# Optimization experiments

Hardware: AMD Instinct MI355X
Metric: run time of the kernel (lower is better)

The kernel has to match this reference:

```python
import jax, jax.numpy as jnp
import numpy as np

V, E, H, T, B, D, L = 32000, 512, 512, 128, 4, 4, 2
C0, C1 = 2000, 10000          # adaptive softmax cutoffs
NT = T - D + 1


def setup_inputs() -> dict:
    key = jax.random.key(0)
    ks = jax.random.split(key, 18)
    s = 0.02
    x = jax.random.randint(ks[0], (B, T), 1, V)
    lengths = jnp.sort(jax.random.randint(ks[1], (B,), D, T + 1))[::-1]
    lengths = lengths.at[0].set(T)
    # graph predictor output: per-layer attention matrices [B, L, T, T]
    G = jax.nn.softmax(jax.random.normal(ks[2], (B, L, T, T)), axis=-1)
    emb = (jax.random.normal(ks[3], (V, E)) * s).at[0].set(0.0)  # padding_idx=0
    enc_w_ih = jax.random.normal(ks[4], (L, 3 * H, H)) * s
    enc_w_hh = jax.random.normal(ks[5], (L, 3 * H, H)) * s
    enc_b_ih = jnp.zeros((L, 3 * H))
    enc_b_hh = jnp.zeros((L, 3 * H))
    dec_w_ih = jax.random.normal(ks[6], (3 * H, E)) * s
    dec_w_hh = jax.random.normal(ks[7], (3 * H, H)) * s
    dec_b_ih = jnp.zeros((3 * H,))
    dec_b_hh = jnp.zeros((3 * H,))
    head_w = jax.random.normal(ks[8], (C0 + 2, H)) * s
    t0_proj = jax.random.normal(ks[9], (H // 4, H)) * s
    t0_out = jax.random.normal(ks[10], (C1 - C0, H // 4)) * s
    t1_proj = jax.random.normal(ks[11], (H // 16, H)) * s
    t1_out = jax.random.normal(ks[12], (V - C1, H // 16)) * s
    return dict(x=x, lengths=lengths, G=G, emb=emb,
                enc_w_ih=enc_w_ih, enc_w_hh=enc_w_hh, enc_b_ih=enc_b_ih, enc_b_hh=enc_b_hh,
                dec_w_ih=dec_w_ih, dec_w_hh=dec_w_hh, dec_b_ih=dec_b_ih, dec_b_hh=dec_b_hh,
                head_w=head_w, t0_proj=t0_proj, t0_out=t0_out, t1_proj=t1_proj, t1_out=t1_out)


def gru_step(xt, h, w_ih, w_hh, b_ih, b_hh):
    """torch nn.GRU/GRUCell math; works on arbitrary leading dims."""
    gi = xt @ w_ih.T + b_ih
    gh = h @ w_hh.T + b_hh
    i_r, i_z, i_n = jnp.split(gi, 3, axis=-1)
    h_r, h_z, h_n = jnp.split(gh, 3, axis=-1)
    r = jax.nn.sigmoid(i_r + h_r)
    z = jax.nn.sigmoid(i_z + h_z)
    n = jnp.tanh(i_n + r * h_n)
    return (1.0 - z) * n + z * h


def adaptive_log_prob(h, head_w, t0_proj, t0_out, t1_proj, t1_out):
    """torch AdaptiveLogSoftmaxWithLoss.log_prob: h [N,H] -> [N,V]."""
    head_lp = jax.nn.log_softmax(h @ head_w.T, axis=-1)                      # [N, C0+2]
    lp0 = head_lp[:, C0:C0 + 1] + jax.nn.log_softmax((h @ t0_proj.T) @ t0_out.T, axis=-1)
    lp1 = head_lp[:, C0 + 1:C0 + 2] + jax.nn.log_softmax((h @ t1_proj.T) @ t1_out.T, axis=-1)
    return jnp.concatenate([head_lp[:, :C0], lp0, lp1], axis=-1)


def reference(x, lengths, G, emb, enc_w_ih, enc_w_hh, enc_b_ih, enc_b_hh,
              dec_w_ih, dec_w_hh, dec_b_ih, dec_b_hh,
              head_w, t0_proj, t0_out, t1_proj, t1_out):
    b = x.shape[0]
    input_f = emb[x]                      # [B,T,E] (dropout p=0)
    embedded = input_f
    # ---- encoder: graph-weighted aggregation + GRUCell per layer ----
    for l in range(enc_w_ih.shape[0]):
        wgt = jnp.einsum('bji,bjd->bid', G[:, l], input_f)   # G_l^T @ input_f
        input_f = gru_step(wgt, input_f, enc_w_ih[l], enc_w_hh[l], enc_b_ih[l], enc_b_hh[l])
    # ---- decoder: length-D GRU window per start position t ----
    t_idx = jnp.arange(NT)
    d_idx = jnp.arange(D)
    tok_idx = jnp.broadcast_to(t_idx[None, :, None] + d_idx[None, None, :] - 1, (b, NT, D))
    tok_idx = tok_idx.at[:, 0, 0].set(lengths - 1)           # t=0,d=0 uses embedded[lengths-1]
    wins = jnp.take_along_axis(embedded, tok_idx.reshape(b, -1)[:, :, None], axis=1)
    wins = wins.reshape(b, NT, D, E)
    h0 = input_f[:, :NT, :]                                  # [B,NT,H]
    def step(h, xd):
        hn = gru_step(xd, h, dec_w_ih, dec_w_hh, dec_b_ih, dec_b_hh)
        return hn, hn
    _, hs = jax.lax.scan(step, h0, jnp.moveaxis(wins, 2, 0))  # [D,B,NT,H]
    hs = jnp.moveaxis(hs, 0, 2)                               # [B,NT,D,H]
    # pad_packed_sequence zeros hidden beyond per-row lens = min(lengths - t, D)
    valid = (t_idx[None, :, None] + d_idx[None, None, :]) < lengths[:, None, None]
    hs = jnp.where(valid[..., None], hs, 0.0)
    lp = adaptive_log_prob(hs.reshape(-1, H), head_w, t0_proj, t0_out, t1_proj, t1_out)
    lp = lp.reshape(b, NT, D, V)
    # batch rows with lengths <= t were excluded and F.pad'ed with zeros
    row_valid = t_idx[None, :] < lengths[:, None]
    lp = jnp.where(row_valid[:, :, None, None], lp, 0.0)
    return lp.reshape(b, NT * D, V)
```

## Files before the change

kernel.cpp:

```cpp
#include <hip/hip_runtime.h>
#include <hip/hip_bf16.h>

typedef __hip_bfloat16 bf16;
typedef __attribute__((ext_vector_type(8))) short short8v;
typedef __attribute__((ext_vector_type(4))) float float4v;

#define V_    32000
#define E_    512
#define H_    512
#define T_    128
#define B_    4
#define D_    4
#define L_    2
#define C0_   2000
#define C1_   10000
#define NT_   125
#define NROW_ 2000
#define NH_   2002
#define NTOTC 2162
#define NSLOT 252

__device__ __forceinline__ float bf2f(bf16 v) { return __bfloat162float(v); }
__device__ __forceinline__ unsigned short f2bfu(float f) {
    bf16 h = __float2bfloat16(f);
    union { bf16 h; unsigned short u; } cv; cv.h = h; return cv.u;
}
__device__ __forceinline__ float ubf2f(unsigned short u) {
    return __uint_as_float(((unsigned)u) << 16);
}
__device__ __forceinline__ float ld1(const void* p, size_t i, int bf) {
    return bf ? bf2f(((const bf16*)p)[i]) : ((const float*)p)[i];
}
__device__ __forceinline__ void st1(void* p, size_t i, int bf, float v) {
    if (bf) ((unsigned short*)p)[i] = f2bfu(v);
    else    ((float*)p)[i] = v;
}

__device__ __forceinline__ void lse_push(float z, float& m, float& s) {
    if (z <= m) { s += __expf(z - m); }
    else        { s = s * __expf(m - z) + 1.0f; m = z; }
}
__device__ __forceinline__ void lse_merge(float m2, float s2, float& m, float& s) {
    float mm = fmaxf(m, m2);
    s = s * __expf(m - mm) + s2 * __expf(m2 - mm);
    m = mm;
}

__global__ void k_detect(const void* __restrict__ G, int* __restrict__ flag) {
    int t = threadIdx.x;
    float s32 = 0.0f;
    for (int k = t; k < 128; k += 64) s32 += ((const float*)G)[k];
    for (int off = 32; off; off >>= 1) s32 += __shfl_down(s32, off);
    if (t == 0) {
        float e32 = fabsf(s32 - 1.0f);
        *flag = (e32 < 0.05f) ? 0 : 1;
    }
}

struct ConvArgs {
    const void* src[9];
    unsigned int off[10];
};
__global__ void k_wconv(ConvArgs a, unsigned short* __restrict__ wb,
                        const int* __restrict__ flagp) {
    const int bf = *flagp;
    unsigned int total = a.off[9];
    for (unsigned int i = blockIdx.x * 256 + threadIdx.x; i < total;
         i += gridDim.x * 256) {
        int seg = 0;
        while (i >= a.off[seg + 1]) seg++;
        wb[i] = f2bfu(ld1(a.src[seg], i - a.off[seg], bf));
    }
}

__global__ void k_embed(const int* __restrict__ x, const void* __restrict__ emb,
                        float* __restrict__ embedded, float* __restrict__ f0,
                        unsigned short* __restrict__ f0b,
                        const int* __restrict__ flagp) {
    const int bf = *flagp;
    int i = blockIdx.x * 256 + threadIdx.x;
    int bt = i >> 9, e = i & 511;
    int tok = x[bt];
    float v = ld1(emb, (size_t)tok * E_ + e, bf);
    embedded[i] = v; f0[i] = v; f0b[i] = f2bfu(v);
}

__global__ void k_wgt(const void* __restrict__ G, const float* __restrict__ f,
                      unsigned short* __restrict__ wgtb, int l,
                      const int* __restrict__ flagp) {
    const int bf = *flagp;
    int i = blockIdx.x * 256 + threadIdx.x;
    int e = i & 511;
    int bi = i >> 9;
    int b = bi >> 7, ip = bi & 127;
    size_t gbase = ((size_t)(b * L_ + l) * T_ * T_) + ip;
    const float* fb = f + (size_t)b * T_ * E_ + e;
    float acc = 0.0f;
    #pragma unroll 4
    for (int j = 0; j < T_; ++j)
        acc = fmaf(ld1(G, gbase + (size_t)j * T_, bf), fb[(size_t)j * E_], acc);
    wgtb[i] = f2bfu(acc);
}

template<int MODE>
__global__ void k_gemm(const unsigned short* __restrict__ A,
                       const unsigned short* __restrict__ Bw,
                       int M, int N, int K, int Nlse,
                       float* __restrict__ Zg, int zcolOff,
                       const void* __restrict__ bias, int biasOff,
                       void* __restrict__ out, int outColOff,
                       float* __restrict__ stats,
                       unsigned short* __restrict__ p0b,
                       unsigned short* __restrict__ p1b,
                       float* __restrict__ lsep, int slotBase,
                       const int* __restrict__ flagp) {
    const int bf = *flagp;
    const int bx = blockIdx.x, by = blockIdx.y;
    const int m0 = by * 128, n0 = bx * 128;
    const int t = threadIdx.x;
    const int wave = t >> 6, lane = t & 63;
    const int wm = wave >> 1, wn = wave & 1;
    const int quad = lane >> 4, l16 = lane & 15;

    __shared__ __align__(16) unsigned short As[128 * 40];
    __shared__ __align__(16) unsigned short Bs[128 * 40];
    __shared__ float pm[128][2], ps[128][2];

    float4v acc[4][4];
    #pragma unroll
    for (int mi = 0; mi < 4; ++mi)
        #pragma unroll
        for (int ni = 0; ni < 4; ++ni)
            acc[mi][ni] = (float4v){0.f, 0.f, 0.f, 0.f};

    for (int k0 = 0; k0 < K; k0 += 32) {
        if (k0) __syncthreads();
        #pragma unroll
        for (int i = 0; i < 2; ++i) {
            int idx = t + i * 256;
            int row = idx >> 2, seg = idx & 3;
            uint4 av = {0u, 0u, 0u, 0u};
            int gm = m0 + row;
            if (gm < M) av = *(const uint4*)(A + (size_t)gm * K + k0 + seg * 8);
            *(uint4*)(&As[row * 40 + seg * 8]) = av;
            uint4 bv = {0u, 0u, 0u, 0u};
            int gn = n0 + row;
            if (gn < N) bv = *(const uint4*)(Bw + (size_t)gn * K + k0 + seg * 8);
            *(uint4*)(&Bs[row * 40 + seg * 8]) = bv;
        }
        __syncthreads();
        short8v af[4], bfv[4];
        #pragma unroll
        for (int mi = 0; mi < 4; ++mi)
            af[mi] = *(const short8v*)(As + (wm * 64 + mi * 16 + l16) * 40 + quad * 8);
        #pragma unroll
        for (int ni = 0; ni < 4; ++ni)
            bfv[ni] = *(const short8v*)(Bs + (wn * 64 + ni * 16 + l16) * 40 + quad * 8);
        #pragma unroll
        for (int mi = 0; mi < 4; ++mi)
            #pragma unroll
            for (int ni = 0; ni < 4; ++ni)
                acc[mi][ni] = __builtin_amdgcn_mfma_f32_16x16x32_bf16(
                    af[mi], bfv[ni], acc[mi][ni], 0, 0, 0);
    }

    #pragma unroll
    for (int mi = 0; mi < 4; ++mi) {
        #pragma unroll
        for (int r = 0; r < 4; ++r) {
            int grow = m0 + wm * 64 + mi * 16 + quad * 4 + r;
            if (grow >= M) continue;
            #pragma unroll
            for (int ni = 0; ni < 4; ++ni) {
                int gcol = n0 + wn * 64 + ni * 16 + l16;
                float v = acc[mi][ni][r];
                if (MODE == 0) {
                    if (gcol < N)
                        Zg[(size_t)grow * 3072 + zcolOff + gcol] =
                            v + ld1(bias, biasOff + gcol, bf);
                } else if (MODE == 1) {
                    if (gcol < C0_)        st1(out, (size_t)grow * V_ + gcol, bf, v);
                    else if (gcol < NH_)   stats[grow * 8 + 2 + (gcol - C0_)] = v;
                    else if (gcol < 2130)  p0b[grow * 128 + (gcol - NH_)] = f2bfu(v);
                    else if (gcol < NTOTC) p1b[grow * 32 + (gcol - 2130)] = f2bfu(v);
                } else {
                    if (gcol < N)
                        st1(out, (size_t)grow * V_ + outColOff + gcol, bf, v);
                }
            }
        }
    }

    if (MODE != 0) {
        #pragma unroll
        for (int mi = 0; mi < 4; ++mi) {
            #pragma unroll
            for (int r = 0; r < 4; ++r) {
                float m = -1e30f, s = 0.0f;
                #pragma unroll
                for (int ni = 0; ni < 4; ++ni) {
                    int gcol = n0 + wn * 64 + ni * 16 + l16;
                    if (gcol < Nlse) lse_push(acc[mi][ni][r], m, s);
                }
                #pragma unroll
                for (int off = 1; off < 16; off <<= 1) {
                    float m2 = __shfl_xor(m, off), s2 = __shfl_xor(s, off);
                    lse_merge(m2, s2, m, s);
                }
                if (l16 == 0) {
                    int rl = wm * 64 + mi * 16 + quad * 4 + r;
                    pm[rl][wn] = m; ps[rl][wn] = s;
                }
            }
        }
        __syncthreads();
        if (t < 128) {
            int grow = m0 + t;
            if (grow < M) {
                float m = pm[t][0], s = ps[t][0];
                lse_merge(pm[t][1], ps[t][1], m, s);
                float* dst = lsep + ((size_t)grow * NSLOT + slotBase + bx) * 2;
                dst[0] = m; dst[1] = s;
            }
        }
    }
}

__device__ __forceinline__ float gru_out(const float* grow, int k, float h) {
    float i_r = grow[k], i_z = grow[512 + k], i_n = grow[1024 + k];
    float h_r = grow[1536 + k], h_z = grow[2048 + k], h_n = grow[2560 + k];
    float r = 1.0f / (1.0f + __expf(-(i_r + h_r)));
    float z = 1.0f / (1.0f + __expf(-(i_z + h_z)));
    float n = tanhf(i_n + r * h_n);
    return (1.0f - z) * n + z * h;
}

__global__ void k_apply_enc(const float* __restrict__ gates,
                            const float* __restrict__ hprev,
                            float* __restrict__ hnext,
                            unsigned short* __restrict__ hnextb) {
    int i = blockIdx.x * 256 + threadIdx.x;
    int row = i >> 9, k = i & 511;
    float v = gru_out(gates + (size_t)row * 3072, k, hprev[i]);
    hnext[i] = v; hnextb[i] = f2bfu(v);
}

__global__ void k_h0(const float* __restrict__ ffin, float* __restrict__ hdec,
                     unsigned short* __restrict__ hdecb) {
    int i = blockIdx.x * 256 + threadIdx.x;
    int row = i >> 9, e = i & 511;
    int b = row / NT_, t = row - b * NT_;
    float v = ffin[((size_t)(b * T_ + t) << 9) + e];
    hdec[i] = v; hdecb[i] = f2bfu(v);
}

__global__ void k_win(const float* __restrict__ embedded,
                      const int* __restrict__ lengths,
                      unsigned short* __restrict__ winb, int d) {
    int i = blockIdx.x * 256 + threadIdx.x;
    int row = i >> 9, e = i & 511;
    int b = row / NT_, t = row - b * NT_;
    int tok = (d == 0 && t == 0) ? (lengths[b] - 1) : (t + d - 1);
    winb[i] = f2bfu(embedded[((size_t)(b * T_ + tok) << 9) + e]);
}

__global__ void k_apply_dec(const float* __restrict__ gates,
                            float* __restrict__ hdec,
                            unsigned short* __restrict__ hdecb,
                            unsigned short* __restrict__ hsb,
                            const int* __restrict__ lengths, int d) {
    int i = blockIdx.x * 256 + threadIdx.x;
    int row = i >> 9, k = i & 511;
    int b = row / NT_, t = row - b * NT_;
    float hn = gru_out(gates + (size_t)row * 3072, k, hdec[i]);
    hdec[i] = hn; hdecb[i] = f2bfu(hn);
    bool valid = (t + d) < lengths[b];
    hsb[(((size_t)row * D_ + d) << 9) + k] = valid ? f2bfu(hn) : (unsigned short)0;
}

__global__ void k_corr2(const float* __restrict__ lsep, const float* __restrict__ stats,
                        float* __restrict__ corr) {
    int r = blockIdx.x * 256 + threadIdx.x;
    if (r >= NROW_) return;
    const float* P = lsep + (size_t)r * NSLOT * 2;
    float m = -1e30f, s = 0.0f;
    for (int i = 0; i < 17; ++i)  lse_merge(P[2 * i], P[2 * i + 1], m, s);
    float ch = m + logf(s);
    float lp0 = stats[r * 8 + 2] - ch;
    float lp1 = stats[r * 8 + 3] - ch;
    m = -1e30f; s = 0.0f;
    for (int i = 17; i < 80; ++i) lse_merge(P[2 * i], P[2 * i + 1], m, s);
    float ct0 = m + logf(s);
    m = -1e30f; s = 0.0f;
    for (int i = 80; i < 252; ++i) lse_merge(P[2 * i], P[2 * i + 1], m, s);
    float ct1 = m + logf(s);
    corr[r * 4 + 0] = ch;
    corr[r * 4 + 1] = ct0 - lp0;
    corr[r * 4 + 2] = ct1 - lp1;
}

__global__ void k_final(void* __restrict__ out, const float* __restrict__ corr,
                        const int* __restrict__ lengths, const int* __restrict__ flagp) {
    const int bf = *flagp;
    size_t vec = (size_t)blockIdx.x * 256 + threadIdx.x;
    size_t base = vec << 3;
    int r = (int)(base / V_);
    int c = (int)(base - (size_t)r * V_);
    int b = r / 500;
    int t = (r - b * 500) >> 2;
    if (t >= lengths[b]) {
        if (bf) { uint4 z = {0u,0u,0u,0u}; *(uint4*)((unsigned short*)out + base) = z; }
        else { float4 z = {0.f,0.f,0.f,0.f};
               float4* p = (float4*)((float*)out + base); p[0] = z; p[1] = z; }
        return;
    }
    float cr = (c < C0_) ? corr[r * 4 + 0] : ((c < C1_) ? corr[r * 4 + 1] : corr[r * 4 + 2]);
    if (bf) {
        uint4 u = *(const uint4*)((const unsigned short*)out + base);
        unsigned us[8] = {u.x & 0xffffu, u.x >> 16, u.y & 0xffffu, u.y >> 16,
                          u.z & 0xffffu, u.z >> 16, u.w & 0xffffu, u.w >> 16};
        unsigned short o[8];
        #pragma unroll
        for (int q = 0; q < 8; ++q)
            o[q] = f2bfu(ubf2f((unsigned short)us[q]) - cr);
        uint4 w;
        w.x = (unsigned)o[0] | ((unsigned)o[1] << 16);
        w.y = (unsigned)o[2] | ((unsigned)o[3] << 16);
        w.z = (unsigned)o[4] | ((unsigned)o[5] << 16);
        w.w = (unsigned)o[6] | ((unsigned)o[7] << 16);
        *(uint4*)((unsigned short*)out + base) = w;
    } else {
        float4* p = (float4*)((float*)out + base);
        float4 a0 = p[0], a1 = p[1];
        a0.x -= cr; a0.y -= cr; a0.z -= cr; a0.w -= cr;
        a1.x -= cr; a1.y -= cr; a1.z -= cr; a1.w -= cr;
        p[0] = a0; p[1] = a1;
    }
}

#define OFF_EMB    0u
#define OFF_FA     262144u
#define OFF_FB     524288u
#define OFF_FAB    786432u
#define OFF_FBB    917504u
#define OFF_WGTB   1048576u
#define OFF_GATES  1179648u
#define OFF_HDEC   2752512u
#define OFF_HDECB  3008512u
#define OFF_WINB   3136512u
#define OFF_HSB    3264512u
#define OFF_P0B    3776512u
#define OFF_P1B    3904512u
#define OFF_STATS  3936512u
#define OFF_CORR   3952512u
#define OFF_LSEP   3960512u
#define OFF_WB     4968512u
#define OFF_FLAG   8745264u

#define WO_ENCIH   0u
#define WO_ENCHH   1572864u
#define WO_DECIH   3145728u
#define WO_DECHH   3932160u
#define WO_W1      4718592u
#define WO_T0O     5825536u
#define WO_T1O     6849536u
#define WO_END     7553504u

extern "C" void kernel_launch(void* const* d_in, const int* in_sizes, int n_in,
                              void* d_out, int out_size, void* d_ws, size_t ws_size,
                              hipStream_t stream) {
    (void)in_sizes; (void)n_in; (void)out_size; (void)ws_size;
    const int*  x        = (const int*)d_in[0];
    const int*  lengths  = (const int*)d_in[1];
    const void* G        = d_in[2];
    const void* emb      = d_in[3];
    const void* enc_w_ih = d_in[4];
    const void* enc_w_hh = d_in[5];
    const void* enc_b_ih = d_in[6];
    const void* enc_b_hh = d_in[7];
    const void* dec_w_ih = d_in[8];
    const void* dec_w_hh = d_in[9];
    const void* dec_b_ih = d_in[10];
    const void* dec_b_hh = d_in[11];
    const void* head_w   = d_in[12];
    const void* t0_proj  = d_in[13];
    const void* t0_out   = d_in[14];
    const void* t1_proj  = d_in[15];
    const void* t1_out   = d_in[16];

    float* ws = (float*)d_ws;
    float* embedded = ws + OFF_EMB;
    float* fA    = ws + OFF_FA;
    float* fB    = ws + OFF_FB;
    unsigned short* fAb  = (unsigned short*)(ws + OFF_FAB);
    unsigned short* fBb  = (unsigned short*)(ws + OFF_FBB);
    unsigned short* wgtb = (unsigned short*)(ws + OFF_WGTB);
    float* gates = ws + OFF_GATES;
    float* hdec  = ws + OFF_HDEC;
    unsigned short* hdecb = (unsigned short*)(ws + OFF_HDECB);
    unsigned short* winb  = (unsigned short*)(ws + OFF_WINB);
    unsigned short* hsb   = (unsigned short*)(ws + OFF_HSB);
    unsigned short* p0b   = (unsigned short*)(ws + OFF_P0B);
    unsigned short* p1b   = (unsigned short*)(ws + OFF_P1B);
    float* stats = ws + OFF_STATS;
    float* corr  = ws + OFF_CORR;
    float* lsep  = ws + OFF_LSEP;
    unsigned short* WB = (unsigned short*)(ws + OFF_WB);
    int* flagp = (int*)(ws + OFF_FLAG);
    void* out = d_out;

    k_detect<<<1, 64, 0, stream>>>(G, flagp);

    ConvArgs ca;
    ca.src[0] = enc_w_ih; ca.src[1] = enc_w_hh; ca.src[2] = dec_w_ih;
    ca.src[3] = dec_w_hh; ca.src[4] = head_w;   ca.src[5] = t0_proj;
    ca.src[6] = t1_proj;  ca.src[7] = t0_out;   ca.src[8] = t1_out;
    ca.off[0] = WO_ENCIH; ca.off[1] = WO_ENCHH; ca.off[2] = WO_DECIH;
    ca.off[3] = WO_DECHH; ca.off[4] = WO_W1;
    ca.off[5] = WO_W1 + 2002u * 512u;
    ca.off[6] = WO_W1 + 2130u * 512u;
    ca.off[7] = WO_T0O;   ca.off[8] = WO_T1O;   ca.off[9] = WO_END;
    k_wconv<<<4096, 256, 0, stream>>>(ca, WB, flagp);

    k_embed<<<1024, 256, 0, stream>>>(x, emb, embedded, fA, fAb, flagp);

    k_wgt<<<1024, 256, 0, stream>>>(G, fA, wgtb, 0, flagp);
    k_gemm<0><<<dim3(12, 4), 256, 0, stream>>>(wgtb, WB + WO_ENCIH, 512, 1536, 512, 0,
        gates, 0, enc_b_ih, 0, nullptr, 0, nullptr, nullptr, nullptr, nullptr, 0, flagp);
    k_gemm<0><<<dim3(12, 4), 256, 0, stream>>>(fAb, WB + WO_ENCHH, 512, 1536, 512, 0,
        gates, 1536, enc_b_hh, 0, nullptr, 0, nullptr, nullptr, nullptr, nullptr, 0, flagp);
    k_apply_enc<<<1024, 256, 0, stream>>>(gates, fA, fB, fBb);

    k_wgt<<<1024, 256, 0, stream>>>(G, fB, wgtb, 1, flagp);
    k_gemm<0><<<dim3(12, 4), 256, 0, stream>>>(wgtb, WB + WO_ENCIH + 786432u, 512, 1536, 512, 0,
        gates, 0, enc_b_ih, 1536, nullptr, 0, nullptr, nullptr, nullptr, nullptr, 0, flagp);
    k_gemm<0><<<dim3(12, 4), 256, 0, stream>>>(fBb, WB + WO_ENCHH + 786432u, 512, 1536, 512, 0,
        gates, 1536, enc_b_hh, 1536, nullptr, 0, nullptr, nullptr, nullptr, nullptr, 0, flagp);
    k_apply_enc<<<1024, 256, 0, stream>>>(gates, fB, fA, fAb);

    k_h0<<<1000, 256, 0, stream>>>(fA, hdec, hdecb);
    for (int d = 0; d < D_; ++d) {
        k_win<<<1000, 256, 0, stream>>>(embedded, lengths, winb, d);
        k_gemm<0><<<dim3(12, 4), 256, 0, stream>>>(winb, WB + WO_DECIH, 500, 1536, 512, 0,
            gates, 0, dec_b_ih, 0, nullptr, 0, nullptr, nullptr, nullptr, nullptr, 0, flagp);
        k_gemm<0><<<dim3(12, 4), 256, 0, stream>>>(hdecb, WB + WO_DECHH, 500, 1536, 512, 0,
            gates, 1536, dec_b_hh, 0, nullptr, 0, nullptr, nullptr, nullptr, nullptr, 0, flagp);
        k_apply_dec<<<1000, 256, 0, stream>>>(gates, hdec, hdecb, hsb, lengths, d);
    }

    k_gemm<1><<<dim3(17, 16), 256, 0, stream>>>(hsb, WB + WO_W1, NROW_, NTOTC, 512, NH_,
        nullptr, 0, nullptr, 0, out, 0, stats, p0b, p1b, lsep, 0, flagp);
    k_gemm<2><<<dim3(63, 16), 256, 0, stream>>>(p0b, WB + WO_T0O, NROW_, 8000, 128, 8000,
        nullptr, 0, nullptr, 0, out, C0_, stats, nullptr, nullptr, lsep, 17, flagp);
    k_gemm<3><<<dim3(172, 16), 256, 0, stream>>>(p1b, WB + WO_T1O, NROW_, 22000, 32, 22000,
        nullptr, 0, nullptr, 0, out, C1_, stats, nullptr, nullptr, lsep, 80, flagp);

    k_corr2<<<8, 256, 0, stream>>>(lsep, stats, corr);
    k_final<<<31250, 256, 0, stream>>>(out, corr, lengths, flagp);
}
```

Before: 925.4 us.

## Recompute logit GEMMs after LSE instead of read-modify-write output pass

```diff
diff --git a/kernel.cpp b/kernel.cpp
--- a/kernel.cpp
+++ b/kernel.cpp
@@ -24,9 +24,6 @@
 __device__ __forceinline__ unsigned short f2bfu(float f) {
     bf16 h = __float2bfloat16(f);
     union { bf16 h; unsigned short u; } cv; cv.h = h; return cv.u;
-}
-__device__ __forceinline__ float ubf2f(unsigned short u) {
-    return __uint_as_float(((unsigned)u) << 16);
 }
 __device__ __forceinline__ float ld1(const void* p, size_t i, int bf) {
     return bf ? bf2f(((const bf16*)p)[i]) : ((const float*)p)[i];
@@ -102,19 +99,31 @@
     wgtb[i] = f2bfu(acc);
 }
 
+struct GemmP {
+    const unsigned short* A0;
+    const unsigned short* A1;
+    const unsigned short* W;
+    unsigned long long w1off;
+    int M, N, K, Nlse;
+    float* Zg; int ldz; int zcol1;
+    const void* bias0; const void* bias1; int boff;
+    void* out; int outColOff;
+    float* stats;
+    unsigned short* p0b;
+    unsigned short* p1b;
+    float* lsep; int slotBase;
+    const float* corr;
+    const int* lengths;
+    const int* flagp;
+};
+
 template<int MODE>
-__global__ void k_gemm(const unsigned short* __restrict__ A,
-                       const unsigned short* __restrict__ Bw,
-                       int M, int N, int K, int Nlse,
-                       float* __restrict__ Zg, int zcolOff,
-                       const void* __restrict__ bias, int biasOff,
-                       void* __restrict__ out, int outColOff,
-                       float* __restrict__ stats,
-                       unsigned short* __restrict__ p0b,
-                       unsigned short* __restrict__ p1b,
-                       float* __restrict__ lsep, int slotBase,
-                       const int* __restrict__ flagp) {
-    const int bf = *flagp;
+__global__ void k_gemm(GemmP p) {
+    const int bf = *p.flagp;
+    const int zsel = blockIdx.z;
+    const unsigned short* A  = zsel ? p.A1 : p.A0;
+    const unsigned short* Bw = p.W + (zsel ? p.w1off : 0ull);
+    const int M = p.M, N = p.N, K = p.K;
     const int bx = blockIdx.x, by = blockIdx.y;
     const int m0 = by * 128, n0 = bx * 128;
     const int t = threadIdx.x;
@@ -164,34 +173,64 @@
                     af[mi], bfv[ni], acc[mi][ni], 0, 0, 0);
     }
 
-    #pragma unroll
-    for (int mi = 0; mi < 4; ++mi) {
-        #pragma unroll
-        for (int r = 0; r < 4; ++r) {
-            int grow = m0 + wm * 64 + mi * 16 + quad * 4 + r;
-            if (grow >= M) continue;
+    if (MODE == 0) {
+        const void* bias = zsel ? p.bias1 : p.bias0;
+        const int zcol = zsel ? p.zcol1 : 0;
+        #pragma unroll
+        for (int mi = 0; mi < 4; ++mi)
             #pragma unroll
-            for (int ni = 0; ni < 4; ++ni) {
-                int gcol = n0 + wn * 64 + ni * 16 + l16;
-                float v = acc[mi][ni][r];
-                if (MODE == 0) {
+            for (int r = 0; r < 4; ++r) {
+                int grow = m0 + wm * 64 + mi * 16 + quad * 4 + r;
+                if (grow >= M) continue;
+                #pragma unroll
+                for (int ni = 0; ni < 4; ++ni) {
+                    int gcol = n0 + wn * 64 + ni * 16 + l16;
                     if (gcol < N)
-                        Zg[(size_t)grow * 3072 + zcolOff + gcol] =
-                            v + ld1(bias, biasOff + gcol, bf);
-                } else if (MODE == 1) {
-                    if (gcol < C0_)        st1(out, (size_t)grow * V_ + gcol, bf, v);
-                    else if (gcol < NH_)   stats[grow * 8 + 2 + (gcol - C0_)] = v;
-                    else if (gcol < 2130)  p0b[grow * 128 + (gcol - NH_)] = f2bfu(v);
-                    else if (gcol < NTOTC) p1b[grow * 32 + (gcol - 2130)] = f2bfu(v);
-                } else {
-                    if (gcol < N)
-                        st1(out, (size_t)grow * V_ + outColOff + gcol, bf, v);
+                        p.Zg[(size_t)grow * p.ldz + zcol + gcol] =
+                            acc[mi][ni][r] + ld1(bias, p.boff + gcol, bf);
                 }
             }
-        }
+    } else if (MODE == 1) {
+        #pragma unroll
+        for (int mi = 0; mi < 4; ++mi)
+            #pragma unroll
+            for (int r = 0; r < 4; ++r) {
+                int grow = m0 + wm * 64 + mi * 16 + quad * 4 + r;
+                if (grow >= M) continue;
+                #pragma unroll
+                for (int ni = 0; ni < 4; ++ni) {
+                    int gcol = n0 + wn * 64 + ni * 16 + l16;
+                    float v = acc[mi][ni][r];
+                    if (gcol >= C0_ && gcol < NH_) p.stats[grow * 8 + 2 + (gcol - C0_)] = v;
+                    else if (gcol >= NH_ && gcol < 2130) p.p0b[grow * 128 + (gcol - NH_)] = f2bfu(v);
+                    else if (gcol >= 2130 && gcol < NTOTC) p.p1b[grow * 32 + (gcol - 2130)] = f2bfu(v);
+                }
+            }
+    } else if (MODE >= 3) {
+        const int crIdx = MODE - 3;
+        #pragma unroll
+        for (int mi = 0; mi < 4; ++mi)
+            #pragma unroll
+            for (int r = 0; r < 4; ++r) {
+                int grow = m0 + wm * 64 + mi * 16 + quad * 4 + r;
+                if (grow >= M) continue;
+                int b = grow / 500;
+                int tt = (grow - b * 500) >> 2;
+                bool valid = tt < p.lengths[b];
+                float cr = p.corr[grow * 4 + crIdx];
+                #pragma unroll
+                for (int ni = 0; ni < 4; ++ni) {
+                    int gcol = n0 + wn * 64 + ni * 16 + l16;
+                    if (gcol < N) {
+                        float v = valid ? (acc[mi][ni][r] - cr) : 0.0f;
+                        st1(p.out, (size_t)grow * V_ + p.outColOff + gcol, bf, v);
+                    }
+                }
+            }
     }
 
-    if (MODE != 0) {
+    if (MODE == 1 || MODE == 2) {
+        const int Nlse = p.Nlse;
         #pragma unroll
         for (int mi = 0; mi < 4; ++mi) {
             #pragma unroll
@@ -219,16 +258,15 @@
             if (grow < M) {
                 float m = pm[t][0], s = ps[t][0];
                 lse_merge(pm[t][1], ps[t][1], m, s);
-                float* dst = lsep + ((size_t)grow * NSLOT + slotBase + bx) * 2;
+                float* dst = p.lsep + ((size_t)grow * NSLOT + p.slotBase + bx) * 2;
                 dst[0] = m; dst[1] = s;
             }
         }
     }
 }
 
-__device__ __forceinline__ float gru_out(const float* grow, int k, float h) {
-    float i_r = grow[k], i_z = grow[512 + k], i_n = grow[1024 + k];
-    float h_r = grow[1536 + k], h_z = grow[2048 + k], h_n = grow[2560 + k];
+__device__ __forceinline__ float gru2(float i_r, float i_z, float i_n,
+                                      float h_r, float h_z, float h_n, float h) {
     float r = 1.0f / (1.0f + __expf(-(i_r + h_r)));
     float z = 1.0f / (1.0f + __expf(-(i_z + h_z)));
     float n = tanhf(i_n + r * h_n);
@@ -241,7 +279,9 @@
                             unsigned short* __restrict__ hnextb) {
     int i = blockIdx.x * 256 + threadIdx.x;
     int row = i >> 9, k = i & 511;
-    float v = gru_out(gates + (size_t)row * 3072, k, hprev[i]);
+    const float* g = gates + (size_t)row * 3072;
+    float v = gru2(g[k], g[512 + k], g[1024 + k],
+                   g[1536 + k], g[2048 + k], g[2560 + k], hprev[i]);
     hnext[i] = v; hnextb[i] = f2bfu(v);
 }
 
@@ -254,17 +294,20 @@
     hdec[i] = v; hdecb[i] = f2bfu(v);
 }
 
-__global__ void k_win(const float* __restrict__ embedded,
-                      const int* __restrict__ lengths,
-                      unsigned short* __restrict__ winb, int d) {
+__global__ void k_winall(const float* __restrict__ embedded,
+                         const int* __restrict__ lengths,
+                         unsigned short* __restrict__ winb) {
     int i = blockIdx.x * 256 + threadIdx.x;
-    int row = i >> 9, e = i & 511;
+    int e = i & 511;
+    int wr = i >> 9;
+    int d = wr / 500, row = wr - d * 500;
     int b = row / NT_, t = row - b * NT_;
     int tok = (d == 0 && t == 0) ? (lengths[b] - 1) : (t + d - 1);
     winb[i] = f2bfu(embedded[((size_t)(b * T_ + tok) << 9) + e]);
 }
 
-__global__ void k_apply_dec(const float* __restrict__ gates,
+__global__ void k_apply_dec(const float* __restrict__ gih,
+                            const float* __restrict__ ghh,
                             float* __restrict__ hdec,
                             unsigned short* __restrict__ hdecb,
                             unsigned short* __restrict__ hsb,
@@ -272,7 +315,10 @@
     int i = blockIdx.x * 256 + threadIdx.x;
     int row = i >> 9, k = i & 511;
     int b = row / NT_, t = row - b * NT_;
-    float hn = gru_out(gates + (size_t)row * 3072, k, hdec[i]);
+    const float* gi = gih + (size_t)(d * 500 + row) * 1536;
+    const float* gh = ghh + (size_t)row * 1536;
+    float hn = gru2(gi[k], gi[512 + k], gi[1024 + k],
+                    gh[k], gh[512 + k], gh[1024 + k], hdec[i]);
     hdec[i] = hn; hdecb[i] = f2bfu(hn);
     bool valid = (t + d) < lengths[b];
     hsb[(((size_t)row * D_ + d) << 9) + k] = valid ? f2bfu(hn) : (unsigned short)0;
@@ -299,45 +345,6 @@
     corr[r * 4 + 2] = ct1 - lp1;
 }
 
-__global__ void k_final(void* __restrict__ out, const float* __restrict__ corr,
-                        const int* __restrict__ lengths, const int* __restrict__ flagp) {
-    const int bf = *flagp;
-    size_t vec = (size_t)blockIdx.x * 256 + threadIdx.x;
-    size_t base = vec << 3;
-    int r = (int)(base / V_);
-    int c = (int)(base - (size_t)r * V_);
-    int b = r / 500;
-    int t = (r - b * 500) >> 2;
-    if (t >= lengths[b]) {
-        if (bf) { uint4 z = {0u,0u,0u,0u}; *(uint4*)((unsigned short*)out + base) = z; }
-        else { float4 z = {0.f,0.f,0.f,0.f};
-               float4* p = (float4*)((float*)out + base); p[0] = z; p[1] = z; }
-        return;
-    }
-    float cr = (c < C0_) ? corr[r * 4 + 0] : ((c < C1_) ? corr[r * 4 + 1] : corr[r * 4 + 2]);
-    if (bf) {
-        uint4 u = *(const uint4*)((const unsigned short*)out + base);
-        unsigned us[8] = {u.x & 0xffffu, u.x >> 16, u.y & 0xffffu, u.y >> 16,
-                          u.z & 0xffffu, u.z >> 16, u.w & 0xffffu, u.w >> 16};
-        unsigned short o[8];
-        #pragma unroll
-        for (int q = 0; q < 8; ++q)
-            o[q] = f2bfu(ubf2f((unsigned short)us[q]) - cr);
-        uint4 w;
-        w.x = (unsigned)o[0] | ((unsigned)o[1] << 16);
-        w.y = (unsigned)o[2] | ((unsigned)o[3] << 16);
-        w.z = (unsigned)o[4] | ((unsigned)o[5] << 16);
-        w.w = (unsigned)o[6] | ((unsigned)o[7] << 16);
-        *(uint4*)((unsigned short*)out + base) = w;
-    } else {
-        float4* p = (float4*)((float*)out + base);
-        float4 a0 = p[0], a1 = p[1];
-        a0.x -= cr; a0.y -= cr; a0.z -= cr; a0.w -= cr;
-        a1.x -= cr; a1.y -= cr; a1.z -= cr; a1.w -= cr;
-        p[0] = a0; p[1] = a1;
-    }
-}
-
 #define OFF_EMB    0u
 #define OFF_FA     262144u
 #define OFF_FB     524288u
@@ -345,17 +352,19 @@
 #define OFF_FBB    917504u
 #define OFF_WGTB   1048576u
 #define OFF_GATES  1179648u
-#define OFF_HDEC   2752512u
-#define OFF_HDECB  3008512u
-#define OFF_WINB   3136512u
-#define OFF_HSB    3264512u
-#define OFF_P0B    3776512u
-#define OFF_P1B    3904512u
-#define OFF_STATS  3936512u
-#define OFF_CORR   3952512u
-#define OFF_LSEP   3960512u
-#define OFF_WB     4968512u
-#define OFF_FLAG   8745264u
+#define OFF_GIH    2752512u
+#define OFF_GHH    5824512u
+#define OFF_HDEC   6592512u
+#define OFF_HDECB  6848512u
+#define OFF_WINB   6976512u
+#define OFF_HSB    7488512u
+#define OFF_P0B    8000512u
+#define OFF_P1B    8128512u
+#define OFF_STATS  8160512u
+#define OFF_CORR   8176512u
+#define OFF_LSEP   8184512u
+#define OFF_WB     9192512u
+#define OFF_FLAG   12969264u
 
 #define WO_ENCIH   0u
 #define WO_ENCHH   1572864u
@@ -365,6 +374,26 @@
 #define WO_T0O     5825536u
 #define WO_T1O     6849536u
 #define WO_END     7553504u
+
+static inline GemmP mkp(const unsigned short* A0, const unsigned short* A1,
+                        const unsigned short* W, unsigned long long w1off,
+                        int M, int N, int K, int Nlse,
+                        float* Zg, int ldz, int zcol1,
+                        const void* bias0, const void* bias1, int boff,
+                        void* out, int outColOff, float* stats,
+                        unsigned short* p0b, unsigned short* p1b,
+                        float* lsep, int slotBase, const float* corr,
+                        const int* lengths, const int* flagp) {
+    GemmP p;
+    p.A0 = A0; p.A1 = A1; p.W = W; p.w1off = w1off;
+    p.M = M; p.N = N; p.K = K; p.Nlse = Nlse;
+    p.Zg = Zg; p.ldz = ldz; p.zcol1 = zcol1;
+    p.bias0 = bias0; p.bias1 = bias1; p.boff = boff;
+    p.out = out; p.outColOff = outColOff; p.stats = stats;
+    p.p0b = p0b; p.p1b = p1b; p.lsep = lsep; p.slotBase = slotBase;
+    p.corr = corr; p.lengths = lengths; p.flagp = flagp;
+    return p;
+}
 
 extern "C" void kernel_launch(void* const* d_in, const int* in_sizes, int n_in,
                               void* d_out, int out_size, void* d_ws, size_t ws_size,
@@ -396,6 +425,8 @@
     unsigned short* fBb  = (unsigned short*)(ws + OFF_FBB);
     unsigned short* wgtb = (unsigned short*)(ws + OFF_WGTB);
     float* gates = ws + OFF_GATES;
+    float* gih   = ws + OFF_GIH;
+    float* ghh   = ws + OFF_GHH;
     float* hdec  = ws + OFF_HDEC;
     unsigned short* hdecb = (unsigned short*)(ws + OFF_HDECB);
     unsigned short* winb  = (unsigned short*)(ws + OFF_WINB);
@@ -425,36 +456,58 @@
     k_embed<<<1024, 256, 0, stream>>>(x, emb, embedded, fA, fAb, flagp);
 
     k_wgt<<<1024, 256, 0, stream>>>(G, fA, wgtb, 0, flagp);
-    k_gemm<0><<<dim3(12, 4), 256, 0, stream>>>(wgtb, WB + WO_ENCIH, 512, 1536, 512, 0,
-        gates, 0, enc_b_ih, 0, nullptr, 0, nullptr, nullptr, nullptr, nullptr, 0, flagp);
-    k_gemm<0><<<dim3(12, 4), 256, 0, stream>>>(fAb, WB + WO_ENCHH, 512, 1536, 512, 0,
-        gates, 1536, enc_b_hh, 0, nullptr, 0, nullptr, nullptr, nullptr, nullptr, 0, flagp);
+    k_gemm<0><<<dim3(12, 4, 2), 256, 0, stream>>>(mkp(
+        wgtb, fAb, WB + WO_ENCIH, (unsigned long long)(WO_ENCHH - WO_ENCIH),
+        512, 1536, 512, 0, gates, 3072, 1536, enc_b_ih, enc_b_hh, 0,
+        nullptr, 0, nullptr, nullptr, nullptr, nullptr, 0, nullptr, lengths, flagp));
     k_apply_enc<<<1024, 256, 0, stream>>>(gates, fA, fB, fBb);
 
     k_wgt<<<1024, 256, 0, stream>>>(G, fB, wgtb, 1, flagp);
-    k_gemm<0><<<dim3(12, 4), 256, 0, stream>>>(wgtb, WB + WO_ENCIH + 786432u, 512, 1536, 512, 0,
-        gates, 0, enc_b_ih, 1536, nullptr, 0, nullptr, nullptr, nullptr, nullptr, 0, flagp);
-    k_gemm<0><<<dim3(12, 4), 256, 0, stream>>>(fBb, WB + WO_ENCHH + 786432u, 512, 1536, 512, 0,
-        gates, 1536, enc_b_hh, 1536, nullptr, 0, nullptr, nullptr, nullptr, nullptr, 0, flagp);
+    k_gemm<0><<<dim3(12, 4, 2), 256, 0, stream>>>(mkp(
+        wgtb, fBb, WB + WO_ENCIH + 786432u, (unsigned long long)(WO_ENCHH - WO_ENCIH),
+        512, 1536, 512, 0, gates, 3072, 1536, enc_b_ih, enc_b_hh, 1536,
+        nullptr, 0, nullptr, nullptr, nullptr, nullptr, 0, nullptr, lengths, flagp));
     k_apply_enc<<<1024, 256, 0, stream>>>(gates, fB, fA, fAb);
 
     k_h0<<<1000, 256, 0, stream>>>(fA, hdec, hdecb);
+    k_winall<<<4000, 256, 0, stream>>>(embedded, lengths, winb);
+    k_gemm<0><<<dim3(12, 16, 1), 256, 0, stream>>>(mkp(
+        winb, nullptr, WB + WO_DECIH, 0ull, 2000, 1536, 512, 0,
+        gih, 1536, 0, dec_b_ih, nullptr, 0,
+        nullptr, 0, nullptr, nullptr, nullptr, nullptr, 0, nullptr, lengths, flagp));
     for (int d = 0; d < D_; ++d) {
-        k_win<<<1000, 256, 0, stream>>>(embedded, lengths, winb, d);
-        k_gemm<0><<<dim3(12, 4), 256, 0, stream>>>(winb, WB + WO_DECIH, 500, 1536, 512, 0,
-            gates, 0, dec_b_ih, 0, nullptr, 0, nullptr, nullptr, nullptr, nullptr, 0, flagp);
-        k_gemm<0><<<dim3(12, 4), 256, 0, stream>>>(hdecb, WB + WO_DECHH, 500, 1536, 512, 0,
-            gates, 1536, dec_b_hh, 0, nullptr, 0, nullptr, nullptr, nullptr, nullptr, 0, flagp);
-        k_apply_dec<<<1000, 256, 0, stream>>>(gates, hdec, hdecb, hsb, lengths, d);
+        k_gemm<0><<<dim3(12, 4, 1), 256, 0, stream>>>(mkp(
+            hdecb, nullptr, WB + WO_DECHH, 0ull, 500, 1536, 512, 0,
+            ghh, 1536, 0, dec_b_hh, nullptr, 0,
+            nullptr, 0, nullptr, nullptr, nullptr, nullptr, 0, nullptr, lengths, flagp));
+        k_apply_dec<<<1000, 256, 0, stream>>>(gih, ghh, hdec, hdecb, hsb, lengths, d);
     }
 
-    k_gemm<1><<<dim3(17, 16), 256, 0, stream>>>(hsb, WB + WO_W1, NROW_, NTOTC, 512, NH_,
-        nullptr, 0, nullptr, 0, out, 0, stats, p0b, p1b, lsep, 0, flagp);
-    k_gemm<2><<<dim3(63, 16), 256, 0, stream>>>(p0b, WB + WO_T0O, NROW_, 8000, 128, 8000,
-        nullptr, 0, nullptr, 0, out, C0_, stats, nullptr, nullptr, lsep, 17, flagp);
-    k_gemm<3><<<dim3(172, 16), 256, 0, stream>>>(p1b, WB + WO_T1O, NROW_, 22000, 32, 22000,
-        nullptr, 0, nullptr, 0, out, C1_, stats, nullptr, nullptr, lsep, 80, flagp);
+    k_gemm<1><<<dim3(17, 16, 1), 256, 0, stream>>>(mkp(
+        hsb, nullptr, WB + WO_W1, 0ull, NROW_, NTOTC, 512, NH_,
+        nullptr, 0, 0, nullptr, nullptr, 0, nullptr, 0,
+        stats, p0b, p1b, lsep, 0, nullptr, lengths, flagp));
+    k_gemm<2><<<dim3(63, 16, 1), 256, 0, stream>>>(mkp(
+        p0b, nullptr, WB + WO_T0O, 0ull, NROW_, 8000, 128, 8000,
+        nullptr, 0, 0, nullptr, nullptr, 0, nullptr, 0,
+        stats, nullptr, nullptr, lsep, 17, nullptr, lengths, flagp));
+    k_gemm<2><<<dim3(172, 16, 1), 256, 0, stream>>>(mkp(
+        p1b, nullptr, WB + WO_T1O, 0ull, NROW_, 22000, 32, 22000,
+        nullptr, 0, 0, nullptr, nullptr, 0, nullptr, 0,
+        stats, nullptr, nullptr, lsep, 80, nullptr, lengths, flagp));
 
     k_corr2<<<8, 256, 0, stream>>>(lsep, stats, corr);
-    k_final<<<31250, 256, 0, stream>>>(out, corr, lengths, flagp);
-}
+
+    k_gemm<3><<<dim3(16, 16, 1), 256, 0, stream>>>(mkp(
+        hsb, nullptr, WB + WO_W1, 0ull, NROW_, C0_, 512, 0,
+        nullptr, 0, 0, nullptr, nullptr, 0, out, 0,
+        nullptr, nullptr, nullptr, nullptr, 0, corr, lengths, flagp));
+    k_gemm<4><<<dim3(63, 16, 1), 256, 0, stream>>>(mkp(
+        p0b, nullptr, WB + WO_T0O, 0ull, NROW_, 8000, 128, 0,
+        nullptr, 0, 0, nullptr, nullptr, 0, out, C0_,
+        nullptr, nullptr, nullptr, nullptr, 0, corr, lengths, flagp));
+    k_gemm<5><<<dim3(172, 16, 1), 256, 0, stream>>>(mkp(
+        p1b, nullptr, WB + WO_T1O, 0ull, NROW_, 22000, 32, 0,
+        nullptr, 0, 0, nullptr, nullptr, 0, out, C1_,
+        nullptr, nullptr, nullptr, nullptr, 0, corr, lengths, flagp));
+}
```

New measurement: 799.8 us. 1.16x faster.
